# Optimization experiments

Measured on AMD Instinct MI355X. Metric: run time of the kernel, lower is better.

The kernel has to match this reference:

```python
import jax, jax.numpy as jnp
import numpy as np

N, IN, HID, OUT, E = 50000, 128, 128, 1, 800000
NEG_SLOPE = 0.2

def setup_inputs() -> dict:
    key = jax.random.key(0)
    ks = jax.random.split(key, 16)
    s = 0.05
    return {
        "x": jax.random.normal(ks[0], (N, IN), jnp.float32),
        "edge_index": jax.random.randint(ks[1], (2, E), 0, N, jnp.int64),
        "W1l": jax.random.normal(ks[2], (IN, HID), jnp.float32) * s,
        "b1l": jnp.zeros((HID,), jnp.float32),
        "W1r": jax.random.normal(ks[3], (IN, HID), jnp.float32) * s,
        "b1r": jnp.zeros((HID,), jnp.float32),
        "att1": jax.random.normal(ks[4], (HID,), jnp.float32) * s,
        "bias1": jnp.zeros((HID,), jnp.float32),
        "W2l": jax.random.normal(ks[5], (HID, OUT), jnp.float32) * s,
        "b2l": jnp.zeros((OUT,), jnp.float32),
        "W2r": jax.random.normal(ks[6], (HID, OUT), jnp.float32) * s,
        "b2r": jnp.zeros((OUT,), jnp.float32),
        "att2": jax.random.normal(ks[7], (OUT,), jnp.float32) * s,
        "bias2": jnp.zeros((OUT,), jnp.float32),
    }

def _gatv2(x, src, dst, Wl, bl, Wr, br, att, bias, n_nodes):
    # GATv2 single-head: e = att . LeakyReLU(Wl x_src + Wr x_dst)
    xl = x @ Wl + bl  # [N, H]
    xr = x @ Wr + br  # [N, H]
    e = jax.nn.leaky_relu(xl[src] + xr[dst], NEG_SLOPE) @ att  # [E]
    m = jax.ops.segment_max(e, dst, num_segments=n_nodes)       # per-dst max
    ex = jnp.exp(e - m[dst])
    denom = jax.ops.segment_sum(ex, dst, num_segments=n_nodes)
    alpha = ex / denom[dst]                                     # neighbor softmax
    out = jax.ops.segment_sum(xl[src] * alpha[:, None], dst, num_segments=n_nodes)
    return out + bias

def reference(x, edge_index, W1l, b1l, W1r, b1r, att1, bias1,
              W2l, b2l, W2r, b2r, att2, bias2):
    n = x.shape[0]
    loops = jnp.arange(n, dtype=edge_index.dtype)
    src = jnp.concatenate([edge_index[0], loops])  # add_self_loops=True
    dst = jnp.concatenate([edge_index[1], loops])
    h = _gatv2(x, src, dst, W1l, b1l, W1r, b1r, att1, bias1, n)
    h = jax.nn.relu(h)
    # dropout is identity at inference (training=False)
    h = _gatv2(h, src, dst, W2l, b2l, W2r, b2r, att2, bias2, n)
    out = jax.nn.sigmoid(h).squeeze()  # [N]
    return (out, out, out)
```

## Files before the change

### kernel.cpp

```cpp
#include <hip/hip_runtime.h>
#include <math.h>

#define NEG_SLOPE 0.2f
#define BCAP 6144

typedef __attribute__((ext_vector_type(8))) short short8;
typedef __attribute__((ext_vector_type(4))) float f32x4;

static __device__ __forceinline__ float lrelu(float t) { return t > 0.f ? t : NEG_SLOPE * t; }
static __device__ __forceinline__ float bf2f(unsigned short h) {
  union { unsigned int i; float f; } c; c.i = ((unsigned int)h) << 16; return c.f;
}
static __device__ __forceinline__ unsigned short f2bf(float x) {
  union { float f; unsigned int i; } c; c.f = x;
  unsigned int r = (c.i + 0x7fffu + ((c.i >> 16) & 1u)) >> 16;
  return (unsigned short)r;
}
static __device__ __forceinline__ void unpack8(uint4 u, float* f) {
  unsigned int d[4] = {u.x, u.y, u.z, u.w};
#pragma unroll
  for (int i = 0; i < 4; ++i) {
    union { unsigned int i_; float f_; } lo, hi;
    lo.i_ = d[i] << 16;
    hi.i_ = d[i] & 0xffff0000u;
    f[2 * i] = lo.f_;
    f[2 * i + 1] = hi.f_;
  }
}

__global__ __launch_bounds__(256) void k_prep(const int* __restrict__ srcI, const int* __restrict__ dstI,
                                              int* __restrict__ gcur, uint2* __restrict__ pairs, int e,
                                              const float* __restrict__ Wl, const float* __restrict__ Wr,
                                              unsigned short* __restrict__ Wth, unsigned short* __restrict__ Wtl) {
  __shared__ int sh[512];
  const int t = threadIdx.x;
  if (blockIdx.x < 512) {
    int* hist = sh;
    int* base = sh + 256;
    int chunk = (e + 511) / 512;
    int lo = blockIdx.x * chunk;
    int hi = lo + chunk; if (hi > e) hi = e;
    hist[t] = 0;
    __syncthreads();
    for (int i = lo + t; i < hi; i += 256) atomicAdd(&hist[dstI[i] >> 8], 1);
    __syncthreads();
    int h = hist[t];
    base[t] = h ? atomicAdd(&gcur[t], h) : 0;
    hist[t] = 0;
    __syncthreads();
    for (int i = lo + t; i < hi; i += 256) {
      int d = dstI[i];
      int b = d >> 8;
      int r = atomicAdd(&hist[b], 1);
      pairs[(size_t)b * BCAP + base[b] + r] = make_uint2((unsigned)d, (unsigned)srcI[i]);
    }
  } else {
    int tid = (blockIdx.x - 512) * 256 + t;
    int wsel = tid >> 14;
    int rem = tid & 16383;
    int k = rem >> 7, c = rem & 127;
    float v = wsel ? Wr[k * 128 + c] : Wl[k * 128 + c];
    unsigned short h = f2bf(v);
    unsigned short lo = f2bf(v - bf2f(h));
    Wth[(c + 128 * wsel) * 128 + k] = h;
    Wtl[(c + 128 * wsel) * 128 + k] = lo;
  }
}

__global__ __launch_bounds__(256) void k_main(const uint2* __restrict__ pairs, const int* __restrict__ gcur,
                                              int* __restrict__ offs, int* __restrict__ csr,
                                              int n, int e, int nbkt,
                                              const float* __restrict__ X,
                                              const unsigned short* __restrict__ Wth,
                                              const unsigned short* __restrict__ Wtl,
                                              const float* __restrict__ bl, const float* __restrict__ br,
                                              const float* __restrict__ att,
                                              unsigned short* __restrict__ xlr,
                                              float* __restrict__ dl, float* __restrict__ dr) {
  __shared__ __align__(16) char lds[40960];
  const int t = threadIdx.x;
  if ((int)blockIdx.x < nbkt) {
    int* cnt = (int*)lds;
    int* pre = cnt + 256;
    int* bb = pre + 256;
    const int b = blockIdx.x;
    bb[t] = (t < nbkt) ? gcur[t] : 0;
    __syncthreads();
    for (int off = 1; off < 256; off <<= 1) {
      int u = (t >= off) ? bb[t - off] : 0;
      __syncthreads();
      bb[t] += u;
      __syncthreads();
    }
    const int mybase = (b == 0) ? 0 : bb[b - 1];
    const int mycnt = bb[b] - mybase;
    const uint2* bp = pairs + (size_t)b * BCAP;
    cnt[t] = 0;
    __syncthreads();
    for (int i = t; i < mycnt; i += 256) atomicAdd(&cnt[bp[i].x & 255], 1);
    __syncthreads();
    pre[t] = cnt[t];
    __syncthreads();
    for (int off = 1; off < 256; off <<= 1) {
      int u = (t >= off) ? pre[t - off] : 0;
      __syncthreads();
      pre[t] += u;
      __syncthreads();
    }
    int d = b * 256 + t;
    if (d < n) offs[d] = mybase + pre[t] - cnt[t];
    if (b == nbkt - 1 && t == 0) offs[n] = e;
    cnt[t] = pre[t] - cnt[t];
    __syncthreads();
    for (int i = t; i < mycnt; i += 256) {
      uint2 pr = bp[i];
      int r = atomicAdd(&cnt[pr.x & 255], 1);
      csr[mybase + r] = (int)pr.y;
    }
    return;
  }
  char* wh = lds;
  char* wlo = lds + 16384;
  char* xh = lds + 32768;
  char* xo = lds + 36864;
  const int w = t >> 6, l = t & 63;
  const int lr = l & 15, lg = l >> 4;
  const int R0 = (blockIdx.x - nbkt) * 64;

  f32x4 acc[4][4];
#pragma unroll
  for (int m = 0; m < 4; ++m)
#pragma unroll
    for (int nn = 0; nn < 4; ++nn) acc[m][nn] = (f32x4)(0.f);

  for (int k0 = 0; k0 < 128; k0 += 32) {
    if (k0) __syncthreads();
#pragma unroll
    for (int i = 0; i < 4; ++i) {
      int flat = t + i * 256;
      int col = flat >> 2, kc = flat & 3;
      int sw = (col & 3) ^ ((col >> 2) & 3);
      int off = col * 64 + ((kc ^ sw) << 4);
      *(uint4*)(wh + off) = *(const uint4*)(Wth + col * 128 + k0 + kc * 8);
      *(uint4*)(wlo + off) = *(const uint4*)(Wtl + col * 128 + k0 + kc * 8);
    }
    {
      int row = t >> 2, kc = t & 3;
      int r = R0 + row;
      float4 v0 = make_float4(0.f, 0.f, 0.f, 0.f), v1 = v0;
      if (r < n) {
        const float* p = X + (size_t)r * 128 + k0 + kc * 8;
        v0 = *(const float4*)p;
        v1 = *(const float4*)(p + 4);
      }
      float xs[8] = {v0.x, v0.y, v0.z, v0.w, v1.x, v1.y, v1.z, v1.w};
      unsigned int hi[4], lo[4];
#pragma unroll
      for (int i = 0; i < 4; ++i) {
        unsigned short h0 = f2bf(xs[2 * i]), h1 = f2bf(xs[2 * i + 1]);
        unsigned short l0 = f2bf(xs[2 * i] - bf2f(h0)), l1 = f2bf(xs[2 * i + 1] - bf2f(h1));
        hi[i] = (unsigned int)h0 | ((unsigned int)h1 << 16);
        lo[i] = (unsigned int)l0 | ((unsigned int)l1 << 16);
      }
      int sw = (row & 3) ^ ((row >> 2) & 3);
      int off = row * 64 + ((kc ^ sw) << 4);
      *(uint4*)(xh + off) = make_uint4(hi[0], hi[1], hi[2], hi[3]);
      *(uint4*)(xo + off) = make_uint4(lo[0], lo[1], lo[2], lo[3]);
    }
    __syncthreads();
    short8 axh[4], axl[4];
#pragma unroll
    for (int m = 0; m < 4; ++m) {
      int row = m * 16 + lr;
      int sw = (row & 3) ^ ((row >> 2) & 3);
      int off = row * 64 + ((lg ^ sw) << 4);
      axh[m] = *(const short8*)(xh + off);
      axl[m] = *(const short8*)(xo + off);
    }
#pragma unroll
    for (int nn = 0; nn < 4; ++nn) {
      int col = w * 64 + nn * 16 + lr;
      int sw = (col & 3) ^ ((col >> 2) & 3);
      int off = col * 64 + ((lg ^ sw) << 4);
      short8 bh = *(const short8*)(wh + off);
      short8 bo = *(const short8*)(wlo + off);
#pragma unroll
      for (int m = 0; m < 4; ++m) {
        acc[m][nn] = __builtin_amdgcn_mfma_f32_16x16x32_bf16(bh, axh[m], acc[m][nn], 0, 0, 0);
        acc[m][nn] = __builtin_amdgcn_mfma_f32_16x16x32_bf16(bh, axl[m], acc[m][nn], 0, 0, 0);
        acc[m][nn] = __builtin_amdgcn_mfma_f32_16x16x32_bf16(bo, axh[m], acc[m][nn], 0, 0, 0);
      }
    }
  }
  __syncthreads();
  float* sred = (float*)lds;
  float part[4];
#pragma unroll
  for (int m = 0; m < 4; ++m) {
    float pm = 0.f;
#pragma unroll
    for (int nn = 0; nn < 4; ++nn) {
      int colb = w * 64 + nn * 16 + lg * 4;
      const float* bp = (colb < 128) ? bl : br;
      float4 bv = *(const float4*)(bp + (colb & 127));
      float4 avv = *(const float4*)(att + (colb & 127));
      f32x4 o = acc[m][nn];
      float v0 = o[0] + bv.x, v1 = o[1] + bv.y, v2 = o[2] + bv.z, v3 = o[3] + bv.w;
      int row = R0 + m * 16 + lr;
      if (row < n) {
        uint2 pk;
        pk.x = (unsigned int)f2bf(v0) | ((unsigned int)f2bf(v1) << 16);
        pk.y = (unsigned int)f2bf(v2) | ((unsigned int)f2bf(v3) << 16);
        *(uint2*)(xlr + (size_t)row * 256 + colb) = pk;
      }
      pm += v0 * avv.x + v1 * avv.y + v2 * avv.z + v3 * avv.w;
    }
    pm += __shfl_xor(pm, 16, 64);
    pm += __shfl_xor(pm, 32, 64);
    part[m] = pm;
  }
  if (lg == 0) {
#pragma unroll
    for (int m = 0; m < 4; ++m) sred[w * 64 + m * 16 + lr] = part[m];
  }
  __syncthreads();
  if (t < 128) {
    int row = t & 63;
    int half = t >> 6;
    if (R0 + row < n) {
      float sum = sred[half * 128 + row] + sred[half * 128 + 64 + row];
      (half ? dr : dl)[R0 + row] = 0.6f * sum;
    }
  }
}

__global__ __launch_bounds__(256) void k_gat1(const unsigned short* __restrict__ xlr,
                                              const float* __restrict__ dl, const float* __restrict__ dr,
                                              const float* __restrict__ att, const float* __restrict__ bias,
                                              const float* __restrict__ W2l, const float* __restrict__ b2l,
                                              const float* __restrict__ W2r, const float* __restrict__ b2r,
                                              const int* __restrict__ offs, const int* __restrict__ csr,
                                              float* __restrict__ hl, float* __restrict__ hr, int n) {
  int wave = (blockIdx.x * 256 + threadIdx.x) >> 6;
  int lane = threadIdx.x & 63;
  if (wave >= n) return;
  const int v = wave;
  const int g = lane >> 4;
  const int q = lane & 15;
  const int cb = q * 8;

  float xrf[8];
  unpack8(*(const uint4*)(xlr + (size_t)v * 256 + 128 + cb), xrf);
  float av[8];
#pragma unroll
  for (int i = 0; i < 8; ++i) av[i] = att[cb + i];
  const float c0 = dr[v];

  float acc[8] = {0.f, 0.f, 0.f, 0.f, 0.f, 0.f, 0.f, 0.f};
  float denom = 0.f;
  const int s0 = offs[v], s1 = offs[v + 1];

  if (g == 0) {
    float dls = dl[v];
    float xf[8];
    unpack8(*(const uint4*)(xlr + (size_t)v * 256 + cb), xf);
    float s2 = 0.f;
#pragma unroll
    for (int i = 0; i < 8; ++i) s2 = fmaf(av[i], fabsf(xf[i] + xrf[i]), s2);
    s2 += __shfl_xor(s2, 1, 64);
    s2 += __shfl_xor(s2, 2, 64);
    s2 += __shfl_xor(s2, 4, 64);
    s2 += __shfl_xor(s2, 8, 64);
    float pe = __expf(fmaf(0.4f, s2, dls + c0));
    denom += pe;
#pragma unroll
    for (int i = 0; i < 8; ++i) acc[i] = fmaf(pe, xf[i], acc[i]);
  }

  for (int j = s0 + g; j < s1; j += 4) {
    int s = csr[j];
    float dls = dl[s];
    float xf[8];
    unpack8(*(const uint4*)(xlr + (size_t)s * 256 + cb), xf);
    float s2 = 0.f;
#pragma unroll
    for (int i = 0; i < 8; ++i) s2 = fmaf(av[i], fabsf(xf[i] + xrf[i]), s2);
    s2 += __shfl_xor(s2, 1, 64);
    s2 += __shfl_xor(s2, 2, 64);
    s2 += __shfl_xor(s2, 4, 64);
    s2 += __shfl_xor(s2, 8, 64);
    float pe = __expf(fmaf(0.4f, s2, dls + c0));
    denom += pe;
#pragma unroll
    for (int i = 0; i < 8; ++i) acc[i] = fmaf(pe, xf[i], acc[i]);
  }
#pragma unroll
  for (int off = 16; off <= 32; off <<= 1) {
#pragma unroll
    for (int i = 0; i < 8; ++i) acc[i] += __shfl_xor(acc[i], off, 64);
    denom += __shfl_xor(denom, off, 64);
  }
  float inv = 1.f / denom;
  float pl = 0.f, pr = 0.f;
#pragma unroll
  for (int i = 0; i < 8; ++i) {
    float h = fmaxf(acc[i] * inv + bias[cb + i], 0.f);
    pl += h * W2l[cb + i];
    pr += h * W2r[cb + i];
  }
#pragma unroll
  for (int off = 1; off <= 8; off <<= 1) {
    pl += __shfl_xor(pl, off, 64);
    pr += __shfl_xor(pr, off, 64);
  }
  if (lane == 0) {
    hl[v] = pl + b2l[0];
    hr[v] = pr + b2r[0];
  }
}

__global__ __launch_bounds__(256) void k_gat2(const float* __restrict__ hl, const float* __restrict__ hr,
                                              const float* __restrict__ att2, const float* __restrict__ bias2,
                                              const int* __restrict__ offs, const int* __restrict__ csr,
                                              float* __restrict__ out, int n) {
  int wave = (blockIdx.x * 256 + threadIdx.x) >> 6;
  int lane = threadIdx.x & 63;
  if (wave >= n) return;
  const int v = wave;
  const float a2 = att2[0];
  const float hrv = hr[v];
  float d = 0.f, num = 0.f;
  if (lane == 0) {
    float hlv = hl[v];
    float pe = __expf(a2 * lrelu(hlv + hrv));
    d += pe;
    num += pe * hlv;
  }
  const int s0 = offs[v], s1 = offs[v + 1];
  for (int j = s0 + lane; j < s1; j += 64) {
    int s = csr[j];
    float hls = hl[s];
    float pe = __expf(a2 * lrelu(hls + hrv));
    d += pe;
    num += pe * hls;
  }
#pragma unroll
  for (int off = 32; off; off >>= 1) {
    d += __shfl_xor(d, off, 64);
    num += __shfl_xor(num, off, 64);
  }
  if (lane == 0) {
    float z = num / d + bias2[0];
    float o = 1.f / (1.f + __expf(-z));
    out[v] = o;
    out[n + v] = o;
    out[2 * n + v] = o;
  }
}

extern "C" void kernel_launch(void* const* d_in, const int* in_sizes, int n_in,
                              void* d_out, int out_size, void* d_ws, size_t ws_size,
                              hipStream_t stream) {
  const float* x     = (const float*)d_in[0];
  const int*   ei    = (const int*)d_in[1];
  const float* W1l   = (const float*)d_in[2];
  const float* b1l   = (const float*)d_in[3];
  const float* W1r   = (const float*)d_in[4];
  const float* b1r   = (const float*)d_in[5];
  const float* att1  = (const float*)d_in[6];
  const float* bias1 = (const float*)d_in[7];
  const float* W2l   = (const float*)d_in[8];
  const float* b2l   = (const float*)d_in[9];
  const float* W2r   = (const float*)d_in[10];
  const float* b2r   = (const float*)d_in[11];
  const float* att2  = (const float*)d_in[12];
  const float* bias2 = (const float*)d_in[13];
  float* out = (float*)d_out;

  const int N = in_sizes[0] / 128;
  const int E = in_sizes[1] / 2;
  const int* srcI = ei;
  const int* dstI = ei + E;
  const int NBKT = (N + 255) >> 8;

  char* w = (char*)d_ws;
  auto alloc = [&](size_t bytes) {
    char* p = w;
    w += (bytes + 255) & ~(size_t)255;
    return p;
  };
  int* gcur  = (int*)alloc(1024);
  uint2* pairs = (uint2*)alloc((size_t)NBKT * BCAP * 8);
  int* offs  = (int*)alloc((size_t)(N + 1) * 4);
  int* csr   = (int*)alloc((size_t)E * 4);
  unsigned short* Wth = (unsigned short*)alloc(256 * 128 * 2);
  unsigned short* Wtl = (unsigned short*)alloc(256 * 128 * 2);
  unsigned short* xlr = (unsigned short*)alloc((size_t)N * 256 * 2);
  float* dl  = (float*)alloc((size_t)N * 4);
  float* dr  = (float*)alloc((size_t)N * 4);
  float* hl  = (float*)alloc((size_t)N * 4);
  float* hr  = (float*)alloc((size_t)N * 4);

  const int LB = (N + 63) / 64;

  hipMemsetAsync(gcur, 0, 1024, stream);
  k_prep<<<640, 256, 0, stream>>>(srcI, dstI, gcur, pairs, E, W1l, W1r, Wth, Wtl);
  k_main<<<NBKT + LB, 256, 0, stream>>>(pairs, gcur, offs, csr, N, E, NBKT,
                                        x, Wth, Wtl, b1l, b1r, att1, xlr, dl, dr);

  const int GB = (N + 3) / 4;
  k_gat1<<<GB, 256, 0, stream>>>(xlr, dl, dr, att1, bias1, W2l, b2l, W2r, b2r, offs, csr, hl, hr, N);
  k_gat2<<<GB, 256, 0, stream>>>(hl, hr, att2, bias2, offs, csr, out, N);
}
```

Baseline: 117.7 us.

## Retune edge bucketing, grid-stride gat1, and quarter-wave-per-node gat2

The edge-bucketing pass now uses many small blocks of 1024 edges and caches each thread's dst/src values in registers, so the scatter phase no longer re-reads the edge arrays. The layer-1 aggregation switches to a fixed 2048-block grid-stride loop, which hoists the attention-vector load out of the per-node loop. The layer-2 aggregation maps 16 lanes per node instead of a whole wave, since average degree is about 16, which cuts idle lanes and launches fewer blocks. The trade-off is more global atomics on the bucket counters from the larger number of prep blocks, and possible load imbalance in the grid-stride loop.

```diff
diff --git a/kernel.cpp b/kernel.cpp
--- a/kernel.cpp
+++ b/kernel.cpp
@@ -29,33 +29,43 @@
 }
 
 __global__ __launch_bounds__(256) void k_prep(const int* __restrict__ srcI, const int* __restrict__ dstI,
-                                              int* __restrict__ gcur, uint2* __restrict__ pairs, int e,
+                                              int* __restrict__ gcur, uint2* __restrict__ pairs, int e, int nbb,
                                               const float* __restrict__ Wl, const float* __restrict__ Wr,
                                               unsigned short* __restrict__ Wth, unsigned short* __restrict__ Wtl) {
-  __shared__ int sh[512];
   const int t = threadIdx.x;
-  if (blockIdx.x < 512) {
-    int* hist = sh;
-    int* base = sh + 256;
-    int chunk = (e + 511) / 512;
-    int lo = blockIdx.x * chunk;
-    int hi = lo + chunk; if (hi > e) hi = e;
+  if ((int)blockIdx.x < nbb) {
+    __shared__ int hist[256];
+    __shared__ int base[256];
+    int lo = blockIdx.x << 10;
+    int hi = lo + 1024; if (hi > e) hi = e;
     hist[t] = 0;
     __syncthreads();
-    for (int i = lo + t; i < hi; i += 256) atomicAdd(&hist[dstI[i] >> 8], 1);
+    int dreg[4], sreg[4];
+    int cnt = 0;
+#pragma unroll
+    for (int u = 0; u < 4; ++u) {
+      int i = lo + u * 256 + t;
+      if (i < hi) {
+        int d = dstI[i];
+        dreg[cnt] = d;
+        sreg[cnt] = srcI[i];
+        atomicAdd(&hist[d >> 8], 1);
+        ++cnt;
+      }
+    }
     __syncthreads();
     int h = hist[t];
     base[t] = h ? atomicAdd(&gcur[t], h) : 0;
     hist[t] = 0;
     __syncthreads();
-    for (int i = lo + t; i < hi; i += 256) {
-      int d = dstI[i];
+    for (int u = 0; u < cnt; ++u) {
+      int d = dreg[u];
       int b = d >> 8;
       int r = atomicAdd(&hist[b], 1);
-      pairs[(size_t)b * BCAP + base[b] + r] = make_uint2((unsigned)d, (unsigned)srcI[i]);
+      pairs[(size_t)b * BCAP + base[b] + r] = make_uint2((unsigned)d, (unsigned)sreg[u]);
     }
   } else {
-    int tid = (blockIdx.x - 512) * 256 + t;
+    int tid = ((int)blockIdx.x - nbb) * 256 + t;
     int wsel = tid >> 14;
     int rem = tid & 16383;
     int k = rem >> 7, c = rem & 127;
@@ -241,81 +251,83 @@
                                               const float* __restrict__ W2r, const float* __restrict__ b2r,
                                               const int* __restrict__ offs, const int* __restrict__ csr,
                                               float* __restrict__ hl, float* __restrict__ hr, int n) {
-  int wave = (blockIdx.x * 256 + threadIdx.x) >> 6;
-  int lane = threadIdx.x & 63;
-  if (wave >= n) return;
-  const int v = wave;
+  const int gw = (blockIdx.x * 256 + threadIdx.x) >> 6;
+  const int nw = (gridDim.x * 256) >> 6;
+  const int lane = threadIdx.x & 63;
   const int g = lane >> 4;
   const int q = lane & 15;
   const int cb = q * 8;
 
-  float xrf[8];
-  unpack8(*(const uint4*)(xlr + (size_t)v * 256 + 128 + cb), xrf);
   float av[8];
 #pragma unroll
   for (int i = 0; i < 8; ++i) av[i] = att[cb + i];
-  const float c0 = dr[v];
-
-  float acc[8] = {0.f, 0.f, 0.f, 0.f, 0.f, 0.f, 0.f, 0.f};
-  float denom = 0.f;
-  const int s0 = offs[v], s1 = offs[v + 1];
-
-  if (g == 0) {
-    float dls = dl[v];
-    float xf[8];
-    unpack8(*(const uint4*)(xlr + (size_t)v * 256 + cb), xf);
-    float s2 = 0.f;
-#pragma unroll
-    for (int i = 0; i < 8; ++i) s2 = fmaf(av[i], fabsf(xf[i] + xrf[i]), s2);
-    s2 += __shfl_xor(s2, 1, 64);
-    s2 += __shfl_xor(s2, 2, 64);
-    s2 += __shfl_xor(s2, 4, 64);
-    s2 += __shfl_xor(s2, 8, 64);
-    float pe = __expf(fmaf(0.4f, s2, dls + c0));
-    denom += pe;
-#pragma unroll
-    for (int i = 0; i < 8; ++i) acc[i] = fmaf(pe, xf[i], acc[i]);
-  }
-
-  for (int j = s0 + g; j < s1; j += 4) {
-    int s = csr[j];
-    float dls = dl[s];
-    float xf[8];
-    unpack8(*(const uint4*)(xlr + (size_t)s * 256 + cb), xf);
-    float s2 = 0.f;
-#pragma unroll
-    for (int i = 0; i < 8; ++i) s2 = fmaf(av[i], fabsf(xf[i] + xrf[i]), s2);
-    s2 += __shfl_xor(s2, 1, 64);
-    s2 += __shfl_xor(s2, 2, 64);
-    s2 += __shfl_xor(s2, 4, 64);
-    s2 += __shfl_xor(s2, 8, 64);
-    float pe = __expf(fmaf(0.4f, s2, dls + c0));
-    denom += pe;
-#pragma unroll
-    for (int i = 0; i < 8; ++i) acc[i] = fmaf(pe, xf[i], acc[i]);
-  }
-#pragma unroll
-  for (int off = 16; off <= 32; off <<= 1) {
-#pragma unroll
-    for (int i = 0; i < 8; ++i) acc[i] += __shfl_xor(acc[i], off, 64);
-    denom += __shfl_xor(denom, off, 64);
-  }
-  float inv = 1.f / denom;
-  float pl = 0.f, pr = 0.f;
-#pragma unroll
-  for (int i = 0; i < 8; ++i) {
-    float h = fmaxf(acc[i] * inv + bias[cb + i], 0.f);
-    pl += h * W2l[cb + i];
-    pr += h * W2r[cb + i];
-  }
-#pragma unroll
-  for (int off = 1; off <= 8; off <<= 1) {
-    pl += __shfl_xor(pl, off, 64);
-    pr += __shfl_xor(pr, off, 64);
-  }
-  if (lane == 0) {
-    hl[v] = pl + b2l[0];
-    hr[v] = pr + b2r[0];
+
+  for (int v = gw; v < n; v += nw) {
+    float xrf[8];
+    unpack8(*(const uint4*)(xlr + (size_t)v * 256 + 128 + cb), xrf);
+    const float c0 = dr[v];
+
+    float acc[8] = {0.f, 0.f, 0.f, 0.f, 0.f, 0.f, 0.f, 0.f};
+    float denom = 0.f;
+    const int s0 = offs[v], s1 = offs[v + 1];
+
+    if (g == 0) {
+      float dls = dl[v];
+      float xf[8];
+      unpack8(*(const uint4*)(xlr + (size_t)v * 256 + cb), xf);
+      float s2 = 0.f;
+#pragma unroll
+      for (int i = 0; i < 8; ++i) s2 = fmaf(av[i], fabsf(xf[i] + xrf[i]), s2);
+      s2 += __shfl_xor(s2, 1, 64);
+      s2 += __shfl_xor(s2, 2, 64);
+      s2 += __shfl_xor(s2, 4, 64);
+      s2 += __shfl_xor(s2, 8, 64);
+      float pe = __expf(fmaf(0.4f, s2, dls + c0));
+      denom += pe;
+#pragma unroll
+      for (int i = 0; i < 8; ++i) acc[i] = fmaf(pe, xf[i], acc[i]);
+    }
+
+    for (int j = s0 + g; j < s1; j += 4) {
+      int s = csr[j];
+      float dls = dl[s];
+      float xf[8];
+      unpack8(*(const uint4*)(xlr + (size_t)s * 256 + cb), xf);
+      float s2 = 0.f;
+#pragma unroll
+      for (int i = 0; i < 8; ++i) s2 = fmaf(av[i], fabsf(xf[i] + xrf[i]), s2);
+      s2 += __shfl_xor(s2, 1, 64);
+      s2 += __shfl_xor(s2, 2, 64);
+      s2 += __shfl_xor(s2, 4, 64);
+      s2 += __shfl_xor(s2, 8, 64);
+      float pe = __expf(fmaf(0.4f, s2, dls + c0));
+      denom += pe;
+#pragma unroll
+      for (int i = 0; i < 8; ++i) acc[i] = fmaf(pe, xf[i], acc[i]);
+    }
+#pragma unroll
+    for (int off = 16; off <= 32; off <<= 1) {
+#pragma unroll
+      for (int i = 0; i < 8; ++i) acc[i] += __shfl_xor(acc[i], off, 64);
+      denom += __shfl_xor(denom, off, 64);
+    }
+    float inv = 1.f / denom;
+    float pl = 0.f, pr = 0.f;
+#pragma unroll
+    for (int i = 0; i < 8; ++i) {
+      float h = fmaxf(acc[i] * inv + bias[cb + i], 0.f);
+      pl += h * W2l[cb + i];
+      pr += h * W2r[cb + i];
+    }
+#pragma unroll
+    for (int off = 1; off <= 8; off <<= 1) {
+      pl += __shfl_xor(pl, off, 64);
+      pr += __shfl_xor(pr, off, 64);
+    }
+    if (lane == 0) {
+      hl[v] = pl + b2l[0];
+      hr[v] = pr + b2r[0];
+    }
   }
 }
 
@@ -325,19 +337,21 @@
                                               float* __restrict__ out, int n) {
   int wave = (blockIdx.x * 256 + threadIdx.x) >> 6;
   int lane = threadIdx.x & 63;
-  if (wave >= n) return;
-  const int v = wave;
+  const int g = lane >> 4;
+  const int q = lane & 15;
+  int v = wave * 4 + g;
+  if (v >= n) return;
   const float a2 = att2[0];
   const float hrv = hr[v];
   float d = 0.f, num = 0.f;
-  if (lane == 0) {
+  if (q == 0) {
     float hlv = hl[v];
     float pe = __expf(a2 * lrelu(hlv + hrv));
     d += pe;
     num += pe * hlv;
   }
   const int s0 = offs[v], s1 = offs[v + 1];
-  for (int j = s0 + lane; j < s1; j += 64) {
+  for (int j = s0 + q; j < s1; j += 16) {
     int s = csr[j];
     float hls = hl[s];
     float pe = __expf(a2 * lrelu(hls + hrv));
@@ -345,11 +359,11 @@
     num += pe * hls;
   }
 #pragma unroll
-  for (int off = 32; off; off >>= 1) {
+  for (int off = 1; off <= 8; off <<= 1) {
     d += __shfl_xor(d, off, 64);
     num += __shfl_xor(num, off, 64);
   }
-  if (lane == 0) {
+  if (q == 0) {
     float z = num / d + bias2[0];
     float o = 1.f / (1.f + __expf(-z));
     out[v] = o;
@@ -382,6 +396,7 @@
   const int* srcI = ei;
   const int* dstI = ei + E;
   const int NBKT = (N + 255) >> 8;
+  const int NBB = (E + 1023) >> 10;
 
   char* w = (char*)d_ws;
   auto alloc = [&](size_t bytes) {
@@ -404,11 +419,11 @@
   const int LB = (N + 63) / 64;
 
   hipMemsetAsync(gcur, 0, 1024, stream);
-  k_prep<<<640, 256, 0, stream>>>(srcI, dstI, gcur, pairs, E, W1l, W1r, Wth, Wtl);
+  k_prep<<<NBB + 128, 256, 0, stream>>>(srcI, dstI, gcur, pairs, E, NBB, W1l, W1r, Wth, Wtl);
   k_main<<<NBKT + LB, 256, 0, stream>>>(pairs, gcur, offs, csr, N, E, NBKT,
                                         x, Wth, Wtl, b1l, b1r, att1, xlr, dl, dr);
 
-  const int GB = (N + 3) / 4;
-  k_gat1<<<GB, 256, 0, stream>>>(xlr, dl, dr, att1, bias1, W2l, b2l, W2r, b2r, offs, csr, hl, hr, N);
-  k_gat2<<<GB, 256, 0, stream>>>(hl, hr, att2, bias2, offs, csr, out, N);
-}
+  k_gat1<<<2048, 256, 0, stream>>>(xlr, dl, dr, att1, bias1, W2l, b2l, W2r, b2r, offs, csr, hl, hr, N);
+  const int GB2 = (N + 15) / 16;
+  k_gat2<<<GB2, 256, 0, stream>>>(hl, hr, att2, bias2, offs, csr, out, N);
+}
```

Result: slower. 135.7 us (+15.3%).
